# Optimization experiments

Hardware: AMD Instinct MI355X
Metric: run time of the kernel (lower is better)

Reference implementation:

```python
import jax, jax.numpy as jnp
import numpy as np

TAU = float(np.exp(-1.0 / 100.0))  # tau_decay default


def setup_inputs() -> dict:
    key = jax.random.key(0)
    k1, k2 = jax.random.split(key)
    x = jax.random.uniform(k1, (16, 128, 64, 64), dtype=jnp.float32)
    W = jax.random.normal(k2, (256, 128, 5, 5), dtype=jnp.float32)
    # normweight(): zero-mean, unit-std per output filter (unbiased=False)
    W = W - W.mean(axis=(1, 2, 3), keepdims=True)
    W = W / W.reshape(W.shape[0], -1).std(axis=1).reshape(-1, 1, 1, 1)
    return {"x": x, "W": W, "T": 8}


def reference(x, W, T):
    # conv2d, no bias, stride 1, padding 2  -> (B, C, H, W)
    y = jax.lax.conv_general_dilated(
        x, W, window_strides=(1, 1), padding=((2, 2), (2, 2)),
        dimension_numbers=("NCHW", "OIHW", "NCHW"))
    # getthresh: per-channel max over (batch, h, w) -> (1, C, 1, 1)
    n = y.max(axis=(0, 2, 3), keepdims=True) + 1e-4
    # clamp + sigmoid-like squash into [0, n)
    y = jnp.clip(y, 0.0)
    y = n / (1.0 + jnp.exp(-(y - 0.4 * n) * (8.0 / n)))

    def step(carry, key):
        mem, xsum = carry
        # LIFSTDPNode: integrate, fire (heaviside), soft reset
        mem = mem * TAU + y
        spike = (mem - n > 0).astype(y.dtype)
        mem = mem * (1.0 - spike)
        # WTA over channel dim with random tie-breaking among spiking units
        r = jax.random.uniform(key, spike.shape, dtype=spike.dtype)
        pos = spike * r
        spike = spike * (pos >= pos.max(axis=1, keepdims=True)).astype(spike.dtype)
        # lateral inhibition, mode='threshold': mem -= threshold * max_c(spike)
        mem = mem - n * spike.max(axis=1, keepdims=True)
        return (mem, xsum + spike), None

    keys = jax.random.split(jax.random.key(42), T)
    init = (jnp.zeros_like(y), jnp.zeros_like(y))
    (_, xsum), _ = jax.lax.scan(step, init, keys)
    return xsum
```

## Files before the change

### kernel.cpp

```cpp
#include <hip/hip_runtime.h>
#include <stdint.h>
#include <math.h>

#define NB  16
#define NCI 128
#define NCO 256
#define NH  64
#define NWD 64

#define Y_ELEMS  (NB*NCO*NH*NWD)

#define NMAX_OFF 0
#define CS_OFF   16384
#define CC_OFF   21504
#define NBUF_OFF 23552
#define YD_OFF   32768
#define YD_BYTES ((size_t)Y_ELEMS*8)
#define XD_OFF   (YD_OFF + YD_BYTES)
#define XD_STRIDE 7168
#define XD_BYTES ((size_t)16*4*68*XD_STRIDE)
#define WD_OFF   (XD_OFF + XD_BYTES)
#define WD_BYTES ((size_t)5*4*25*8192)
#define WS_NEED  (WD_OFF + WD_BYTES)

struct Keys { uint32_t a[8]; uint32_t b[8]; };

typedef int v4i  __attribute__((ext_vector_type(4)));
typedef int v16i __attribute__((ext_vector_type(16)));

typedef __attribute__((address_space(1))) const void* gas_t;
typedef __attribute__((address_space(3))) void*       las_t;

__host__ __device__ inline void threefry2x32(uint32_t k0, uint32_t k1,
                                             uint32_t x0, uint32_t x1,
                                             uint32_t* o0, uint32_t* o1)
{
  uint32_t ks2 = k0 ^ k1 ^ 0x1BD11BDAu;
  x0 += k0; x1 += k1;
#define TF_R(r) { x0 += x1; x1 = (x1 << (r)) | (x1 >> (32 - (r))); x1 ^= x0; }
  TF_R(13) TF_R(15) TF_R(26) TF_R(6)
  x0 += k1;  x1 += ks2 + 1u;
  TF_R(17) TF_R(29) TF_R(16) TF_R(24)
  x0 += ks2; x1 += k0 + 2u;
  TF_R(13) TF_R(15) TF_R(26) TF_R(6)
  x0 += k0;  x1 += k1 + 3u;
  TF_R(17) TF_R(29) TF_R(16) TF_R(24)
  x0 += k1;  x1 += ks2 + 4u;
  TF_R(13) TF_R(15) TF_R(26) TF_R(6)
  x0 += ks2; x1 += k0 + 5u;
#undef TF_R
  *o0 = x0; *o1 = x1;
}

__device__ inline unsigned long long dkey(double d)
{
  unsigned long long b = (unsigned long long)__double_as_longlong(d);
  return (b & 0x8000000000000000ULL) ? ~b : (b | 0x8000000000000000ULL);
}

__global__ void init_kernel(unsigned long long* nmax, int* cs)
{
  #pragma unroll
  for (int i = 0; i < 8; ++i) nmax[i * 256 + threadIdx.x] = 0ull;
  #pragma unroll
  for (int j = 0; j < 5; ++j) cs[j * 256 + threadIdx.x] = 0;
}

__global__ __launch_bounds__(256) void xdigit_kernel(const float* __restrict__ x,
                                                     signed char* __restrict__ xd)
{
  __shared__ __align__(16) signed char l[6912];
  const int row = blockIdx.x;
  const int g   = blockIdx.y;
  const int b   = blockIdx.z;
  for (int o = threadIdx.x; o < 2304; o += 256) {
    int cl = o / 72, col = o - (o / 72) * 72;
    int r = row - 2, cc = col - 2;
    float v = 0.f;
    if ((unsigned)r < 64u && (unsigned)cc < 64u)
      v = x[(((size_t)b * 128 + g * 32 + cl) * 64 + r) * 64 + cc];
    unsigned long long X = (unsigned long long)((double)v * 1099511627776.0);
    const int p = col * 32 + cl;
    l[p]        = (signed char)((int)((X >> 16) & 255u) - 128);
    l[2304 + p] = (signed char)((int)((X >> 24) & 255u) - 128);
    l[4608 + p] = (signed char)((int)((X >> 32) & 255u) - 128);
  }
  __syncthreads();
  uint4* dst = (uint4*)(xd + ((size_t)(b * 4 + g) * 68 + row) * XD_STRIDE);
  const uint4* src = (const uint4*)l;
  for (int o = threadIdx.x; o < 432; o += 256) dst[o] = src[o];
}

__global__ __launch_bounds__(256) void wdigit_kernel(const float* __restrict__ W,
                                                     signed char* __restrict__ wd,
                                                     int* __restrict__ cs)
{
  const int g = blockIdx.x, tap = blockIdx.y, co = threadIdx.x;
  __attribute__((aligned(16))) signed char db[5][32];
  for (int c = 0; c < 32; ++c) {
    float w = W[((size_t)co * 128 + g * 32 + c) * 25 + tap];
    long long q = __double2ll_rn((double)w * 68719476736.0);
    #pragma unroll
    for (int j = 0; j < 5; ++j) {
      int d = (int)(q & 255);
      if (d >= 128) d -= 256;
      q = (q - d) >> 8;
      db[j][c] = (signed char)d;
    }
  }
  #pragma unroll
  for (int j = 0; j < 5; ++j) {
    size_t off = (((size_t)j * 4 + g) * 25 + tap) * 8192 + (size_t)co * 32;
    *(uint4*)(wd + off)      = *(const uint4*)(&db[j][0]);
    *(uint4*)(wd + off + 16) = *(const uint4*)(&db[j][16]);
    int s = 0;
    #pragma unroll
    for (int c = 0; c < 32; ++c) s += (int)db[j][c];
    atomicAdd(&cs[j * 256 + co], s);
  }
}

__global__ void ccorr_kernel(const int* __restrict__ cs, double* __restrict__ cc)
{
  const int co = threadIdx.x;
  const double K0 = 0x1.0p-44;
  const double K1 = 0x1.0p-44 + 0x1.0p-36;
  const double K2 = 0x1.0p-44 + 0x1.0p-36 + 0x1.0p-28;
  const double K3 = 0x1.0p-36 + 0x1.0p-28 + 0x1.0p-20;
  const double K4 = 0x1.0p-28 + 0x1.0p-20 + 0x1.0p-12;
  double C = (double)cs[co]           * K0
           + (double)cs[256 + co]     * K1
           + (double)cs[512 + co]     * K2
           + (double)cs[768 + co]     * K3
           + (double)cs[1024 + co]    * K4;
  cc[co] = 128.0 * C;
}

__global__ __launch_bounds__(256, 3) void ozconv_kernel(const signed char* __restrict__ xd,
                                                        const signed char* __restrict__ wd,
                                                        const double* __restrict__ cc,
                                                        double* __restrict__ yd,
                                                        unsigned long long* __restrict__ nmax)
{
  __shared__ __align__(16) signed char A[2 * XD_STRIDE];

  const int sid = (blockIdx.x & 7) * 512 + (blockIdx.x >> 3);
  const int cog = sid >> 10;
  const int b   = (sid >> 6) & 15;
  const int h0  = sid & 63;

  const int tid  = threadIdx.x;
  const int lane = tid & 63, wv = tid >> 6;
  const int wm = wv & 1, wn = wv >> 1;
  const int l31 = lane & 31, kg = lane >> 5;
  const int co0 = cog * 64;
  const int b4  = b * 4;
  const int colbase = 32 * wm + l31;

  v16i acc[5] = {};

  auto stage = [&](int t, int bs) {
    int g = t / 5, kh = t - 5 * (t / 5);
    const signed char* src = xd + ((size_t)(b4 + g) * 68 + (h0 + kh)) * XD_STRIDE + lane * 16;
    signed char* dst = &A[bs * XD_STRIDE];
    for (int c = wv; c < 7; c += 4)
      __builtin_amdgcn_global_load_lds((gas_t)(const void*)(src + c * 1024),
                                       (las_t)(void*)(dst + c * 1024), 16, 0, 0);
  };

  stage(0, 0);
  asm volatile("s_waitcnt vmcnt(0)" ::: "memory");
  __syncthreads();

  const size_t coff = (size_t)(co0 + 32 * wn + l31) * 32 + 16 * kg;

  #pragma unroll 1
  for (int t = 0; t < 20; ++t) {
    if (t < 19) stage(t + 1, (t + 1) & 1);

    const int g = t / 5, kh = t - 5 * (t / 5);
    const signed char* Ab = &A[(t & 1) * XD_STRIDE];
    const signed char* wbase = wd + ((size_t)(g * 25 + kh * 5)) * 8192 + coff;

    #pragma unroll 1
    for (int kw = 0; kw < 5; ++kw) {
      const int aoff = (colbase + kw) * 32 + kg * 16;
      v4i a[3];
      #pragma unroll
      for (int i = 0; i < 3; ++i)
        a[i] = *(const v4i*)(Ab + i * 2304 + aoff);
      v4i bf[5];
      #pragma unroll
      for (int j = 0; j < 5; ++j)
        bf[j] = *(const v4i*)(wbase + (size_t)j * 819200 + kw * 8192);

      #pragma unroll
      for (int p = 0; p < 5; ++p) {
        const int j = 4 - p;
        #pragma unroll
        for (int i = 0; i < 3; ++i) {
          const int s = i + j - 2;
          if (s >= 0)
            acc[s] = __builtin_amdgcn_mfma_i32_32x32x32_i8(a[i], bf[j], acc[s], 0, 0, 0);
        }
      }
    }

    asm volatile("s_waitcnt vmcnt(0)" ::: "memory");
    __syncthreads();
  }

  const double S[5] = {0x1.0p-44, 0x1.0p-36, 0x1.0p-28, 0x1.0p-20, 0x1.0p-12};
  const int co = co0 + 32 * wn + l31;
  const double C = cc[co];
  const size_t base = (((size_t)b * 64 + h0) * 64) * 256 + co;
  double lmax = -1.0e300;
  #pragma unroll
  for (int r = 0; r < 16; ++r) {
    int row = (r & 3) + 8 * (r >> 2) + 4 * kg;
    int w   = 32 * wm + row;
    double y = C;
    #pragma unroll
    for (int s = 0; s < 5; ++s) y = fma((double)acc[s][r], S[s], y);
    yd[base + (size_t)w * 256] = y;
    lmax = fmax(lmax, y);
  }
  lmax = fmax(lmax, __shfl_xor(lmax, 32));
  if (kg == 0)
    atomicMax(&nmax[co * 8 + (blockIdx.x & 7)], dkey(lmax));
}

__global__ void n_kernel(const unsigned long long* __restrict__ nmax,
                         double* __restrict__ nbuf)
{
  int c = threadIdx.x;
  unsigned long long u = 0ull;
  #pragma unroll
  for (int i = 0; i < 8; ++i) {
    unsigned long long v = nmax[c * 8 + i];
    u = v > u ? v : u;
  }
  unsigned long long bits = (u & 0x8000000000000000ULL) ? (u ^ 0x8000000000000000ULL) : ~u;
  double m = __longlong_as_double((long long)bits);
  nbuf[c] = m + 1e-4;
}

__global__ __launch_bounds__(256) void dyn_kernel(const double* __restrict__ yd,
                                                  const double* __restrict__ nbuf,
                                                  float* __restrict__ out,
                                                  Keys K, double tau)
{
  const int tid  = threadIdx.x;
  const int lane = tid & 63;
  const int wv   = tid >> 6;
  const int pix  = blockIdx.x * 4 + wv;
  const int b    = pix >> 12;
  const int hw   = pix & 4095;
  const int c0   = lane * 4;

  double y[4], n[4];
  {
    const double* yp = yd + (size_t)pix * 256 + c0;
    #pragma unroll
    for (int q = 0; q < 4; ++q) {
      n[q] = nbuf[c0 + q];
      double yraw = yp[q];
      double yc = yraw > 0.0 ? yraw : 0.0;
      y[q] = n[q] / (1.0 + exp(-((yc - 0.4 * n[q]) * (8.0 / n[q]))));
    }
  }

  double mem[4]; float xs[4];
  #pragma unroll
  for (int q = 0; q < 4; ++q) { mem[q] = y[q]; xs[q] = 0.f; }

  const uint32_t ebase = (uint32_t)((b * 256 + c0) * 4096 + hw);

  #pragma unroll 1
  for (int t = 1; t < 8; ++t) {
    double m[4]; bool sp[4]; float pos[4];
    #pragma unroll
    for (int q = 0; q < 4; ++q) {
      m[q]  = mem[q] * tau + y[q];
      sp[q] = (m[q] - n[q]) > 0.0;
    }
    float lmax = 0.f;
    #pragma unroll
    for (int q = 0; q < 4; ++q) {
      float r = 0.f;
      if (__any(sp[q])) {
        uint32_t o0, o1;
        threefry2x32(K.a[t], K.b[t], 0u, ebase + (uint32_t)(q * 4096), &o0, &o1);
        uint32_t ub = ((o0 ^ o1) >> 9) | 0x3f800000u;
        r = __uint_as_float(ub) - 1.0f;
      }
      pos[q] = sp[q] ? r : 0.f;
      lmax = fmaxf(lmax, pos[q]);
    }
    float pmax = lmax;
    #pragma unroll
    for (int o = 32; o > 0; o >>= 1) pmax = fmaxf(pmax, __shfl_xor(pmax, o));

    bool anyl = false;
    float s2[4];
    #pragma unroll
    for (int q = 0; q < 4; ++q) {
      s2[q] = (sp[q] && pos[q] >= pmax) ? 1.f : 0.f;
      anyl |= (s2[q] != 0.f);
    }
    float smax = __any(anyl) ? 1.f : 0.f;

    #pragma unroll
    for (int q = 0; q < 4; ++q) {
      mem[q] = (sp[q] ? 0.0 : m[q]) - n[q] * (double)smax;
      xs[q] += s2[q];
    }
  }

  const size_t ob = ((size_t)b * 256 + c0) * 4096 + hw;
  #pragma unroll
  for (int q = 0; q < 4; ++q)
    out[ob + (size_t)q * 4096] = xs[q];
}

extern "C" void kernel_launch(void* const* d_in, const int* in_sizes, int n_in,
                              void* d_out, int out_size, void* d_ws, size_t ws_size,
                              hipStream_t stream)
{
  const float* x = (const float*)d_in[0];
  const float* W = (const float*)d_in[1];

  if (ws_size < WS_NEED) return;

  char* ws = (char*)d_ws;
  unsigned long long* nmax = (unsigned long long*)(ws + NMAX_OFF);
  int*                cs   = (int*)(ws + CS_OFF);
  double*             cc   = (double*)(ws + CC_OFF);
  double*             nbuf = (double*)(ws + NBUF_OFF);
  double*             yd   = (double*)(ws + YD_OFF);
  signed char*        xd   = (signed char*)(ws + XD_OFF);
  signed char*        wdp  = (signed char*)(ws + WD_OFF);

  float* out = (float*)d_out;

  init_kernel<<<1, 256, 0, stream>>>(nmax, cs);
  xdigit_kernel<<<dim3(68, 4, 16), 256, 0, stream>>>(x, xd);
  wdigit_kernel<<<dim3(4, 25), 256, 0, stream>>>(W, wdp, cs);
  ccorr_kernel<<<1, 256, 0, stream>>>(cs, cc);
  ozconv_kernel<<<4096, 256, 0, stream>>>(xd, wdp, cc, yd, nmax);
  n_kernel<<<1, 256, 0, stream>>>(nmax, nbuf);

  Keys K;
  for (int t = 0; t < 8; ++t) {
    uint32_t a, b;
    threefry2x32(0u, 42u, 0u, (uint32_t)t, &a, &b);
    K.a[t] = a; K.b[t] = b;
  }
  double tau = exp(-0.01);

  dyn_kernel<<<NB * NH * NWD / 4, 256, 0, stream>>>(yd, nbuf, out, K, tau);
}
```

Baseline: 736.0 us.

## Stage two input rows per barrier and software-prefetch weight fragments

Each pipeline step now stages two kh rows into LDS instead of one, which halves the number of barrier and waitcnt points across the 20 row steps and doubles the LDS buffer. The weight fragments for the next kw tap are loaded from global memory one iteration ahead, so their latency can overlap the current MFMA batch. The cost is higher register pressure from the extra bfn set, which may lower occupancy under launch_bounds(256,3), and double the LDS footprint per block.

```diff
diff --git a/kernel.cpp b/kernel.cpp
--- a/kernel.cpp
+++ b/kernel.cpp
@@ -128,11 +128,11 @@
   const double K2 = 0x1.0p-44 + 0x1.0p-36 + 0x1.0p-28;
   const double K3 = 0x1.0p-36 + 0x1.0p-28 + 0x1.0p-20;
   const double K4 = 0x1.0p-28 + 0x1.0p-20 + 0x1.0p-12;
-  double C = (double)cs[co]           * K0
-           + (double)cs[256 + co]     * K1
-           + (double)cs[512 + co]     * K2
-           + (double)cs[768 + co]     * K3
-           + (double)cs[1024 + co]    * K4;
+  double C = (double)cs[co]        * K0
+           + (double)cs[256 + co]  * K1
+           + (double)cs[512 + co]  * K2
+           + (double)cs[768 + co]  * K3
+           + (double)cs[1024 + co] * K4;
   cc[co] = 128.0 * C;
 }
 
@@ -142,7 +142,7 @@
                                                         double* __restrict__ yd,
                                                         unsigned long long* __restrict__ nmax)
 {
-  __shared__ __align__(16) signed char A[2 * XD_STRIDE];
+  __shared__ __align__(16) signed char A[2 * 2 * XD_STRIDE];
 
   const int sid = (blockIdx.x & 7) * 512 + (blockIdx.x >> 3);
   const int cog = sid >> 10;
@@ -159,50 +159,78 @@
 
   v16i acc[5] = {};
 
-  auto stage = [&](int t, int bs) {
-    int g = t / 5, kh = t - 5 * (t / 5);
-    const signed char* src = xd + ((size_t)(b4 + g) * 68 + (h0 + kh)) * XD_STRIDE + lane * 16;
-    signed char* dst = &A[bs * XD_STRIDE];
-    for (int c = wv; c < 7; c += 4)
-      __builtin_amdgcn_global_load_lds((gas_t)(const void*)(src + c * 1024),
-                                       (las_t)(void*)(dst + c * 1024), 16, 0, 0);
+  auto stage2 = [&](int p, int bs) {
+    #pragma unroll
+    for (int rr = 0; rr < 2; ++rr) {
+      const int t = 2 * p + rr;
+      const int g = t / 5, kh = t - 5 * (t / 5);
+      const signed char* src = xd + ((size_t)(b4 + g) * 68 + (h0 + kh)) * XD_STRIDE + lane * 16;
+      signed char* dst = &A[(bs * 2 + rr) * XD_STRIDE];
+      for (int c = wv; c < 7; c += 4)
+        __builtin_amdgcn_global_load_lds((gas_t)(const void*)(src + c * 1024),
+                                         (las_t)(void*)(dst + c * 1024), 16, 0, 0);
+    }
   };
 
-  stage(0, 0);
+  stage2(0, 0);
   asm volatile("s_waitcnt vmcnt(0)" ::: "memory");
   __syncthreads();
 
   const size_t coff = (size_t)(co0 + 32 * wn + l31) * 32 + 16 * kg;
 
   #pragma unroll 1
-  for (int t = 0; t < 20; ++t) {
-    if (t < 19) stage(t + 1, (t + 1) & 1);
-
-    const int g = t / 5, kh = t - 5 * (t / 5);
-    const signed char* Ab = &A[(t & 1) * XD_STRIDE];
-    const signed char* wbase = wd + ((size_t)(g * 25 + kh * 5)) * 8192 + coff;
-
-    #pragma unroll 1
-    for (int kw = 0; kw < 5; ++kw) {
+  for (int p = 0; p < 10; ++p) {
+    if (p < 9) stage2(p + 1, (p + 1) & 1);
+
+    const int t0 = 2 * p, t1 = t0 + 1;
+    const int g0 = t0 / 5, kh0 = t0 - 5 * (t0 / 5);
+    const int g1 = t1 / 5, kh1 = t1 - 5 * (t1 / 5);
+    const signed char* Ab0 = &A[((p & 1) * 2) * XD_STRIDE];
+    const signed char* Ab1 = Ab0 + XD_STRIDE;
+    const signed char* wb0 = wd + ((size_t)(g0 * 25 + kh0 * 5)) * 8192 + coff;
+    const signed char* wb1 = wd + ((size_t)(g1 * 25 + kh1 * 5)) * 8192 + coff;
+
+    v4i bfc[5];
+    #pragma unroll
+    for (int j = 0; j < 5; ++j)
+      bfc[j] = *(const v4i*)(wb0 + (size_t)j * 819200);
+
+    #pragma unroll 2
+    for (int s = 0; s < 10; ++s) {
+      const int r  = (s >= 5) ? 1 : 0;
+      const int kw = s - 5 * r;
+      const signed char* Ar = r ? Ab1 : Ab0;
       const int aoff = (colbase + kw) * 32 + kg * 16;
       v4i a[3];
       #pragma unroll
       for (int i = 0; i < 3; ++i)
-        a[i] = *(const v4i*)(Ab + i * 2304 + aoff);
-      v4i bf[5];
+        a[i] = *(const v4i*)(Ar + i * 2304 + aoff);
+
+      v4i bfn[5];
+      if (s < 9) {
+        const int s1 = s + 1;
+        const int r1 = (s1 >= 5) ? 1 : 0;
+        const int k1 = s1 - 5 * r1;
+        const signed char* wbn = r1 ? wb1 : wb0;
+        #pragma unroll
+        for (int j = 0; j < 5; ++j)
+          bfn[j] = *(const v4i*)(wbn + (size_t)j * 819200 + (size_t)k1 * 8192);
+      }
+
       #pragma unroll
-      for (int j = 0; j < 5; ++j)
-        bf[j] = *(const v4i*)(wbase + (size_t)j * 819200 + kw * 8192);
-
-      #pragma unroll
-      for (int p = 0; p < 5; ++p) {
-        const int j = 4 - p;
+      for (int q = 0; q < 5; ++q) {
+        const int j = 4 - q;
         #pragma unroll
         for (int i = 0; i < 3; ++i) {
-          const int s = i + j - 2;
-          if (s >= 0)
-            acc[s] = __builtin_amdgcn_mfma_i32_32x32x32_i8(a[i], bf[j], acc[s], 0, 0, 0);
+          const int ss = i + j - 2;
+          if (ss >= 0)
+            acc[ss] = __builtin_amdgcn_mfma_i32_32x32x32_i8(a[i], bfc[j], acc[ss], 0, 0, 0);
         }
+      }
+
+      if (s < 9) {
+        #pragma unroll
+        for (int j = 0; j < 5; ++j) bfc[j] = bfn[j];
       }
     }
 
```

Measured after the change: 754.6 us. 1.03x slower.

## Load conv input fragments directly from global with register double-buffering instead of LDS

Applied to the files above, without the earlier changes.

The ozconv kernel no longer stages input rows into shared memory with global_load_lds and per-row barriers. Each wave now reads its A and B fragments straight from global memory into registers and prefetches the next kw step's fragments while the current MFMAs run, with the kw loop fully unrolled. This removes the LDS traffic and the __syncthreads per row and overlaps loads with compute. In exchange it uses more registers for the second fragment set and relies on L1/L2 to absorb the repeated global reads that LDS sharing used to serve.

```diff
diff --git a/kernel.cpp b/kernel.cpp
--- a/kernel.cpp
+++ b/kernel.cpp
@@ -27,9 +27,6 @@
 
 typedef int v4i  __attribute__((ext_vector_type(4)));
 typedef int v16i __attribute__((ext_vector_type(16)));
-
-typedef __attribute__((address_space(1))) const void* gas_t;
-typedef __attribute__((address_space(3))) void*       las_t;
 
 __host__ __device__ inline void threefry2x32(uint32_t k0, uint32_t k1,
                                              uint32_t x0, uint32_t x1,
@@ -128,11 +125,11 @@
   const double K2 = 0x1.0p-44 + 0x1.0p-36 + 0x1.0p-28;
   const double K3 = 0x1.0p-36 + 0x1.0p-28 + 0x1.0p-20;
   const double K4 = 0x1.0p-28 + 0x1.0p-20 + 0x1.0p-12;
-  double C = (double)cs[co]           * K0
-           + (double)cs[256 + co]     * K1
-           + (double)cs[512 + co]     * K2
-           + (double)cs[768 + co]     * K3
-           + (double)cs[1024 + co]    * K4;
+  double C = (double)cs[co]        * K0
+           + (double)cs[256 + co]  * K1
+           + (double)cs[512 + co]  * K2
+           + (double)cs[768 + co]  * K3
+           + (double)cs[1024 + co] * K4;
   cc[co] = 128.0 * C;
 }
 
@@ -142,8 +139,6 @@
                                                         double* __restrict__ yd,
                                                         unsigned long long* __restrict__ nmax)
 {
-  __shared__ __align__(16) signed char A[2 * XD_STRIDE];
-
   const int sid = (blockIdx.x & 7) * 512 + (blockIdx.x >> 3);
   const int cog = sid >> 10;
   const int b   = (sid >> 6) & 15;
@@ -159,55 +154,67 @@
 
   v16i acc[5] = {};
 
-  auto stage = [&](int t, int bs) {
-    int g = t / 5, kh = t - 5 * (t / 5);
-    const signed char* src = xd + ((size_t)(b4 + g) * 68 + (h0 + kh)) * XD_STRIDE + lane * 16;
-    signed char* dst = &A[bs * XD_STRIDE];
-    for (int c = wv; c < 7; c += 4)
-      __builtin_amdgcn_global_load_lds((gas_t)(const void*)(src + c * 1024),
-                                       (las_t)(void*)(dst + c * 1024), 16, 0, 0);
+  int aoff[5];
+  #pragma unroll
+  for (int kw = 0; kw < 5; ++kw) aoff[kw] = (colbase + kw) * 32 + 16 * kg;
+  const int boff = (co0 + 32 * wn + l31) * 32 + 16 * kg;
+
+  auto arow_ptr = [&](int t) {
+    const int g = t / 5, kh = t - 5 * (t / 5);
+    return xd + ((size_t)(b4 + g) * 68 + (h0 + kh)) * XD_STRIDE;
   };
-
-  stage(0, 0);
-  asm volatile("s_waitcnt vmcnt(0)" ::: "memory");
-  __syncthreads();
-
-  const size_t coff = (size_t)(co0 + 32 * wn + l31) * 32 + 16 * kg;
+  auto wrow_ptr = [&](int t) {
+    const int g = t / 5, kh = t - 5 * (t / 5);
+    return wd + (size_t)(g * 25 + kh * 5) * 8192 + boff;
+  };
+
+  const signed char* arow_c = arow_ptr(0);
+  const signed char* wrow_c = wrow_ptr(0);
+  v4i a_c[3], b_c[5];
+  #pragma unroll
+  for (int i = 0; i < 3; ++i) a_c[i] = *(const v4i*)(arow_c + i * 2304 + aoff[0]);
+  #pragma unroll
+  for (int j = 0; j < 5; ++j) b_c[j] = *(const v4i*)(wrow_c + (size_t)j * 819200);
 
   #pragma unroll 1
   for (int t = 0; t < 20; ++t) {
-    if (t < 19) stage(t + 1, (t + 1) & 1);
-
-    const int g = t / 5, kh = t - 5 * (t / 5);
-    const signed char* Ab = &A[(t & 1) * XD_STRIDE];
-    const signed char* wbase = wd + ((size_t)(g * 25 + kh * 5)) * 8192 + coff;
-
-    #pragma unroll 1
+    const signed char* arow_n = (t < 19) ? arow_ptr(t + 1) : arow_c;
+    const signed char* wrow_n = (t < 19) ? wrow_ptr(t + 1) : wrow_c;
+
+    #pragma unroll
     for (int kw = 0; kw < 5; ++kw) {
-      const int aoff = (colbase + kw) * 32 + kg * 16;
-      v4i a[3];
+      v4i a_n[3], b_n[5];
+      const bool last = (t == 19) && (kw == 4);
+      if (!last) {
+        const signed char* ar  = (kw < 4) ? arow_c : arow_n;
+        const signed char* wr  = (kw < 4) ? wrow_c : wrow_n;
+        const int kwn = (kw < 4) ? kw + 1 : 0;
+        #pragma unroll
+        for (int i = 0; i < 3; ++i) a_n[i] = *(const v4i*)(ar + i * 2304 + aoff[kwn]);
+        #pragma unroll
+        for (int j = 0; j < 5; ++j) b_n[j] = *(const v4i*)(wr + (size_t)j * 819200 + (size_t)kwn * 8192);
+      }
+
       #pragma unroll
-      for (int i = 0; i < 3; ++i)
-        a[i] = *(const v4i*)(Ab + i * 2304 + aoff);
-      v4i bf[5];
-      #pragma unroll
-      for (int j = 0; j < 5; ++j)
-        bf[j] = *(const v4i*)(wbase + (size_t)j * 819200 + kw * 8192);
-
-      #pragma unroll
-      for (int p = 0; p < 5; ++p) {
-        const int j = 4 - p;
+      for (int q = 0; q < 5; ++q) {
+        const int j = 4 - q;
         #pragma unroll
         for (int i = 0; i < 3; ++i) {
-          const int s = i + j - 2;
-          if (s >= 0)
-            acc[s] = __builtin_amdgcn_mfma_i32_32x32x32_i8(a[i], bf[j], acc[s], 0, 0, 0);
+          const int ss = i + j - 2;
+          if (ss >= 0)
+            acc[ss] = __builtin_amdgcn_mfma_i32_32x32x32_i8(a_c[i], b_c[j], acc[ss], 0, 0, 0);
         }
       }
-    }
-
-    asm volatile("s_waitcnt vmcnt(0)" ::: "memory");
-    __syncthreads();
+
+      if (!last) {
+        #pragma unroll
+        for (int i = 0; i < 3; ++i) a_c[i] = a_n[i];
+        #pragma unroll
+        for (int j = 0; j < 5; ++j) b_c[j] = b_n[j];
+      }
+    }
+    arow_c = arow_n;
+    wrow_c = wrow_n;
   }
 
   const double S[5] = {0x1.0p-44, 0x1.0p-36, 0x1.0p-28, 0x1.0p-20, 0x1.0p-12};
```

After: 813.7 us. 10.6% more time.
